# Kernel optimization log

Hardware: AMD Instinct MI355X
Metric: run time of the kernel (lower is better)

Reference implementation:

```python
import jax, jax.numpy as jnp
import numpy as np

B, S, HID = 1, 4096, 1024
NH, HD = 16, 64            # heads, per-head dim
BS = 256                    # block size
PB = 256                    # position buckets (= max_relative_positions)
EPS = 1e-7


def make_log_bucket_position(rel, num_buckets, max_position):
    sign = jnp.sign(rel)
    max_exact = num_buckets // 2
    in_exact = (rel < max_exact) & (rel > -max_exact)
    abs_pos = jnp.where(in_exact, max_exact - 1, jnp.abs(rel))
    x = jnp.log((max_position - 1) / max_exact)
    xx = jnp.log(abs_pos / max_exact) / x
    log_pos = jnp.ceil(xx * (max_exact - 1)) + max_exact
    return jnp.where(abs_pos <= max_exact, rel, (log_pos * sign).astype(jnp.int32)).astype(jnp.int32)


def split_into_blocks(x, block_size, axis):
    # [..., S, ...] -> [..., S//bs, bs, ...]; S assumed divisible by bs
    shp = x.shape
    new = shp[:axis] + (shp[axis] // block_size, block_size) + shp[axis + 1:]
    return x.reshape(new)


def concat_3_blocks(x, block_axis, seq_axis, pad_value=0):
    # pad one zero block on each side of the block axis, then concat
    # [prev, cur, next] along the within-block seq axis.
    pad = [(0, 0)] * x.ndim
    pad[block_axis] = (1, 1)
    xp = jnp.pad(x, pad, constant_values=pad_value)
    nb = x.shape[block_axis]
    slices = [jax.lax.dynamic_slice_in_dim(xp, i, nb, block_axis) for i in range(3)]
    return jnp.concatenate(slices, axis=seq_axis)


def layer_norm(x, scale, bias):
    mu = jnp.mean(x, axis=-1, keepdims=True)
    var = jnp.mean(jnp.square(x - mu), axis=-1, keepdims=True)
    return (x - mu) * jax.lax.rsqrt(var + EPS) * scale + bias


def setup_inputs() -> dict:
    key = jax.random.key(0)
    ks = jax.random.split(key, 8)
    d = {
        'hidden_states': jax.random.normal(ks[0], (B, S, HID), jnp.float32) * 0.02,
        'rel_pos_embeddings': jax.random.normal(ks[1], (S, HID), jnp.float32) * 0.02,
        'Wq': jax.random.normal(ks[2], (HID, HID), jnp.float32) * 0.01,
        'bq': jnp.zeros((HID,), jnp.float32),
        'Wk': jax.random.normal(ks[3], (HID, HID), jnp.float32) * 0.01,
        'bk': jnp.zeros((HID,), jnp.float32),
        'Wv': jax.random.normal(ks[4], (HID, HID), jnp.float32) * 0.01,
        'bv': jnp.zeros((HID,), jnp.float32),
        'Wo': jax.random.normal(ks[5], (HID, HID), jnp.float32) * 0.01,
        'bo': jnp.zeros((HID,), jnp.float32),
        'ln_scale': jnp.ones((HID,), jnp.float32),
        'ln_bias': jnp.zeros((HID,), jnp.float32),
    }
    return d


def reference(hidden_states, rel_pos_embeddings, Wq, bq, Wk, bk, Wv, bv, Wo, bo, ln_scale, ln_bias):
    b, s, hid = hidden_states.shape

    def heads(x):
        return x.reshape(x.shape[:-1] + (NH, HD))

    # content projections -> [B, nb, bs, h, d]
    q = split_into_blocks(heads(hidden_states @ Wq + bq), BS, axis=1)
    k = split_into_blocks(heads(hidden_states @ Wk + bk), BS, axis=1)
    v = split_into_blocks(heads(hidden_states @ Wv + bv), BS, axis=1)
    k3 = concat_3_blocks(k, block_axis=1, seq_axis=2)   # [B, nb, 3bs, h, d]
    v3 = concat_3_blocks(v, block_axis=1, seq_axis=2)

    c2c = jnp.einsum('bnqhd,bnkhd->bnhqk', q, k3)

    # position projections, stacked over batch (size-1 batch dim broadcasts in einsum)
    pos_q = split_into_blocks(heads(rel_pos_embeddings @ Wq + bq)[None], BS, axis=1)  # [1, nb, bs, h, d]
    pos_k = split_into_blocks(heads(rel_pos_embeddings @ Wk + bk)[None], BS, axis=1)
    pos_k3 = concat_3_blocks(pos_k, block_axis=1, seq_axis=2)                          # [1, nb, 3bs, h, d]

    rel = jnp.arange(BS, dtype=jnp.int32)[:, None] - jnp.arange(3 * BS, dtype=jnp.int32)[None, :]
    rel = make_log_bucket_position(rel, PB, PB)
    idx = jnp.clip(rel + PB, 0, 2 * PB - 1)            # [bs, 3bs]

    c2p = jnp.einsum('bnqhd,bnkhd->bnhqk', q, pos_k3)  # [B, nb, h, bs, 3bs]
    # faithful to the source: axis-less jnp.take gathers from the FLATTENED
    # score tensor -> [bs, 3bs] bias broadcast over (batch, block, head)
    c2p_bias = jnp.take(c2p, idx)

    p2c = jnp.einsum('bnqhd,bnkhd->bnhqk', pos_q, k3)
    p2c_bias = jnp.take(p2c, idx)

    scale = jnp.sqrt(jnp.asarray(HD * 3, hidden_states.dtype))
    attn = (c2c + c2p_bias + p2c_bias) / scale
    probs = jax.nn.softmax(attn, axis=-1)

    ctx = jnp.einsum('bnhqk,bnkhd->bnqhd', probs, v3)  # [B, nb, bs, h, d]
    ctx = ctx.reshape(b, s, hid)
    out = ctx @ Wo + bo
    return layer_norm(out + hidden_states, ln_scale, ln_bias)
```

## Files before the change

kernel.cpp:

```cpp
#include <hip/hip_runtime.h>
#include <stdint.h>

typedef unsigned short u16;
typedef __bf16 bf16_t;
typedef bf16_t v8bf __attribute__((ext_vector_type(8)));
typedef float v4f __attribute__((ext_vector_type(4)));

#define SEQ   4096
#define HIDN  1024
#define NHEAD 16
#define HDIM  64
#define BLK   256
#define NBLK  16

#define GLOAD_LDS16(g, l) __builtin_amdgcn_global_load_lds( \
  (const __attribute__((address_space(1))) unsigned*)(g), \
  (__attribute__((address_space(3))) unsigned*)(l), 16, 0, 0)

__device__ __forceinline__ u16 f2bf(float f){
  union { __bf16 b; u16 u; } v; v.b = (__bf16)f;
  return v.u;
}
__device__ __forceinline__ float bf2f(u16 h){
  union { unsigned u; float f; } v; v.u = ((unsigned)h) << 16;
  return v.f;
}
__device__ __forceinline__ unsigned packbf(float a, float b){
  unsigned r;
  asm("v_cvt_pk_bf16_f32 %0, %1, %2" : "=v"(r) : "v"(a), "v"(b));
  return r;
}

__global__ __launch_bounds__(256) void k_prep(const float* __restrict__ hidden, u16* __restrict__ hb,
    const float* __restrict__ Wq, const float* __restrict__ Wk,
    const float* __restrict__ Wv, const float* __restrict__ Wo, u16* __restrict__ Wt,
    const float* __restrict__ bq, const float* __restrict__ bk, const float* __restrict__ bv,
    float* __restrict__ bcat,
    const float* __restrict__ rpe, float* __restrict__ posk, float* __restrict__ posq0)
{
  __shared__ float t[32][33];
  __shared__ float red[4][64];
  int b = blockIdx.x, tid = threadIdx.x;
  if (b < 4096){
    int w = b >> 10, tile = b & 1023;
    int k0 = (tile & 31) * 32, n0 = (tile >> 5) * 32;
    const float* W = (w == 0) ? Wq : (w == 1) ? Wk : (w == 2) ? Wv : Wo;
    u16* outp = Wt + (size_t)w * 1024 * 1024;
    int x = tid & 31, y = tid >> 5;
    #pragma unroll
    for (int yy = 0; yy < 32; yy += 8) t[y + yy][x] = W[(size_t)(k0 + y + yy) * 1024 + n0 + x];
    __syncthreads();
    #pragma unroll
    for (int yy = 0; yy < 32; yy += 8) outp[(size_t)(n0 + y + yy) * 1024 + k0 + x] = f2bf(t[x][y + yy]);
  } else if (b < 4608){
    int base = (b - 4096) * 8192;
    #pragma unroll
    for (int j = 0; j < 8; j++){
      int i = base + j * 1024 + tid * 4;
      float4 f = *(const float4*)&hidden[i];
      uint2 p; p.x = packbf(f.x, f.y); p.y = packbf(f.z, f.w);
      *(uint2*)&hb[i] = p;
    }
  } else if (b == 4608){
    #pragma unroll
    for (int j = 0; j < 12; j++){
      int i = j * 256 + tid;
      const float* src = i < 1024 ? bq : (i < 2048 ? bk : bv);
      bcat[i] = src[i & 1023];
    }
  } else {
    int pb = b - 4609;
    int d = tid & 63, part = tid >> 6;
    const float* W  = (pb < 256) ? Wk : Wq;
    const float* rv = (pb < 256) ? &rpe[(size_t)pb * 1024] : rpe;
    float s = 0.f;
    for (int k = part * 256; k < part * 256 + 256; k++) s += rv[k] * W[(size_t)k * 1024 + d];
    red[part][d] = s;
    __syncthreads();
    if (part == 0){
      s = red[0][d] + red[1][d] + red[2][d] + red[3][d];
      if (pb < 256) posk[pb * 64 + d] = s + bk[d];
      else          posq0[d] = s + bq[d];
    }
  }
}

__global__ __launch_bounds__(256) void k_gemm_qkv(const u16* __restrict__ A, const u16* __restrict__ Bt,
                                                  const float* __restrict__ bias,
                                                  u16* __restrict__ qk, u16* __restrict__ Vt)
{
  __shared__ alignas(16) u16 As[2][128 * 32];
  __shared__ alignas(16) u16 Bs[2][128 * 32];
  int tid = threadIdx.x, lane = tid & 63, wid = tid >> 6;
  int wr = wid >> 1, wc = wid & 1;
  int m0 = blockIdx.y * 128, n0 = blockIdx.x * 128;
  const int K = 1024;

  v4f acc[4][4];
  #pragma unroll
  for (int m = 0; m < 4; m++)
    #pragma unroll
    for (int n = 0; n < 4; n++) acc[m][n] = (v4f){0.f, 0.f, 0.f, 0.f};

  int r = lane & 15, g = lane >> 4;
  int ob0 = wid * 2048;
  int o0  = ob0 + lane * 16;
  int row0 = o0 >> 6, col0 = (o0 & 63) >> 1;
  int row1 = (o0 + 1024) >> 6, col1 = ((o0 + 1024) & 63) >> 1;

  GLOAD_LDS16(&A [(size_t)(m0 + row0) * K + col0], &As[0][ob0 >> 1]);
  GLOAD_LDS16(&Bt[(size_t)(n0 + row0) * K + col0], &Bs[0][ob0 >> 1]);
  GLOAD_LDS16(&A [(size_t)(m0 + row1) * K + col1], &As[0][(ob0 + 1024) >> 1]);
  GLOAD_LDS16(&Bt[(size_t)(n0 + row1) * K + col1], &Bs[0][(ob0 + 1024) >> 1]);
  __syncthreads();

  int cur = 0;
  for (int kt = 0; kt < K - 32; kt += 32){
    int nx = cur ^ 1, kn = kt + 32;
    GLOAD_LDS16(&A [(size_t)(m0 + row0) * K + kn + col0], &As[nx][ob0 >> 1]);
    GLOAD_LDS16(&Bt[(size_t)(n0 + row0) * K + kn + col0], &Bs[nx][ob0 >> 1]);
    GLOAD_LDS16(&A [(size_t)(m0 + row1) * K + kn + col1], &As[nx][(ob0 + 1024) >> 1]);
    GLOAD_LDS16(&Bt[(size_t)(n0 + row1) * K + kn + col1], &Bs[nx][(ob0 + 1024) >> 1]);

    v8bf a[4], bb[4];
    #pragma unroll
    for (int m = 0; m < 4; m++) a[m] = *(const v8bf*)&As[cur][(wr * 64 + m * 16 + r) * 32 + g * 8];
    #pragma unroll
    for (int n = 0; n < 4; n++) bb[n] = *(const v8bf*)&Bs[cur][(wc * 64 + n * 16 + r) * 32 + g * 8];
    #pragma unroll
    for (int m = 0; m < 4; m++)
      #pragma unroll
      for (int n = 0; n < 4; n++)
        acc[m][n] = __builtin_amdgcn_mfma_f32_16x16x32_bf16(a[m], bb[n], acc[m][n], 0, 0, 0);
    __syncthreads();
    cur = nx;
  }
  {
    v8bf a[4], bb[4];
    #pragma unroll
    for (int m = 0; m < 4; m++) a[m] = *(const v8bf*)&As[cur][(wr * 64 + m * 16 + r) * 32 + g * 8];
    #pragma unroll
    for (int n = 0; n < 4; n++) bb[n] = *(const v8bf*)&Bs[cur][(wc * 64 + n * 16 + r) * 32 + g * 8];
    #pragma unroll
    for (int m = 0; m < 4; m++)
      #pragma unroll
      for (int n = 0; n < 4; n++)
        acc[m][n] = __builtin_amdgcn_mfma_f32_16x16x32_bf16(a[m], bb[n], acc[m][n], 0, 0, 0);
  }

  #pragma unroll
  for (int m = 0; m < 4; m++)
    #pragma unroll
    for (int n = 0; n < 4; n++){
      int col = n0 + wc * 64 + n * 16 + r;
      float bv = bias[col];
      if (n0 < 2048){
        #pragma unroll
        for (int i = 0; i < 4; i++){
          int row = m0 + wr * 64 + m * 16 + g * 4 + i;
          qk[(size_t)row * 2048 + col] = f2bf(acc[m][n][i] + bv);
        }
      } else {
        uint2 pk;
        pk.x = packbf(acc[m][n][0] + bv, acc[m][n][1] + bv);
        pk.y = packbf(acc[m][n][2] + bv, acc[m][n][3] + bv);
        int row = m0 + wr * 64 + m * 16 + g * 4;
        *(uint2*)&Vt[(size_t)(col - 2048) * 4096 + row] = pk;
      }
    }
}

__global__ __launch_bounds__(256) void k_gemm_out(const u16* __restrict__ A, const u16* __restrict__ Bt,
                                                  const float* __restrict__ bias,
                                                  const float* __restrict__ resid, float* __restrict__ Cout)
{
  __shared__ alignas(16) u16 As[2][128 * 32];
  __shared__ alignas(16) u16 Bs[2][128 * 32];
  int tid = threadIdx.x, lane = tid & 63, wid = tid >> 6;
  int wr = wid >> 1, wc = wid & 1;
  int m0 = blockIdx.y * 128, n0 = blockIdx.x * 128;
  const int K = 1024;

  v4f acc[4][4];
  #pragma unroll
  for (int m = 0; m < 4; m++)
    #pragma unroll
    for (int n = 0; n < 4; n++) acc[m][n] = (v4f){0.f, 0.f, 0.f, 0.f};

  int r = lane & 15, g = lane >> 4;
  int ob0 = wid * 2048;
  int o0  = ob0 + lane * 16;
  int row0 = o0 >> 6, col0 = (o0 & 63) >> 1;
  int row1 = (o0 + 1024) >> 6, col1 = ((o0 + 1024) & 63) >> 1;

  GLOAD_LDS16(&A [(size_t)(m0 + row0) * K + col0], &As[0][ob0 >> 1]);
  GLOAD_LDS16(&Bt[(size_t)(n0 + row0) * K + col0], &Bs[0][ob0 >> 1]);
  GLOAD_LDS16(&A [(size_t)(m0 + row1) * K + col1], &As[0][(ob0 + 1024) >> 1]);
  GLOAD_LDS16(&Bt[(size_t)(n0 + row1) * K + col1], &Bs[0][(ob0 + 1024) >> 1]);
  __syncthreads();

  int cur = 0;
  for (int kt = 0; kt < K - 32; kt += 32){
    int nx = cur ^ 1, kn = kt + 32;
    GLOAD_LDS16(&A [(size_t)(m0 + row0) * K + kn + col0], &As[nx][ob0 >> 1]);
    GLOAD_LDS16(&Bt[(size_t)(n0 + row0) * K + kn + col0], &Bs[nx][ob0 >> 1]);
    GLOAD_LDS16(&A [(size_t)(m0 + row1) * K + kn + col1], &As[nx][(ob0 + 1024) >> 1]);
    GLOAD_LDS16(&Bt[(size_t)(n0 + row1) * K + kn + col1], &Bs[nx][(ob0 + 1024) >> 1]);

    v8bf a[4], bb[4];
    #pragma unroll
    for (int m = 0; m < 4; m++) a[m] = *(const v8bf*)&As[cur][(wr * 64 + m * 16 + r) * 32 + g * 8];
    #pragma unroll
    for (int n = 0; n < 4; n++) bb[n] = *(const v8bf*)&Bs[cur][(wc * 64 + n * 16 + r) * 32 + g * 8];
    #pragma unroll
    for (int m = 0; m < 4; m++)
      #pragma unroll
      for (int n = 0; n < 4; n++)
        acc[m][n] = __builtin_amdgcn_mfma_f32_16x16x32_bf16(a[m], bb[n], acc[m][n], 0, 0, 0);
    __syncthreads();
    cur = nx;
  }
  {
    v8bf a[4], bb[4];
    #pragma unroll
    for (int m = 0; m < 4; m++) a[m] = *(const v8bf*)&As[cur][(wr * 64 + m * 16 + r) * 32 + g * 8];
    #pragma unroll
    for (int n = 0; n < 4; n++) bb[n] = *(const v8bf*)&Bs[cur][(wc * 64 + n * 16 + r) * 32 + g * 8];
    #pragma unroll
    for (int m = 0; m < 4; m++)
      #pragma unroll
      for (int n = 0; n < 4; n++)
        acc[m][n] = __builtin_amdgcn_mfma_f32_16x16x32_bf16(a[m], bb[n], acc[m][n], 0, 0, 0);
  }

  #pragma unroll
  for (int m = 0; m < 4; m++)
    #pragma unroll
    for (int n = 0; n < 4; n++){
      int col = n0 + wc * 64 + n * 16 + r;
      float bv = bias[col];
      #pragma unroll
      for (int i = 0; i < 4; i++){
        int row = m0 + wr * 64 + m * 16 + g * 4 + i;
        Cout[(size_t)row * 1024 + col] = acc[m][n][i] + bv + resid[(size_t)row * 1024 + col];
      }
    }
}

__global__ __launch_bounds__(256) void k_brow(const u16* __restrict__ qk,
                                              const float* __restrict__ posk, const float* __restrict__ posq0,
                                              float* __restrict__ brow)
{
  int b = blockIdx.x, tid = threadIdx.x;
  if (tid < 32) brow[b * 32 + tid] = 0.f;
  int u = b * 32 + (tid >> 3), sub = tid & 7;
  float c2p = 0.f, p2c = 0.f;
  #pragma unroll
  for (int j = 0; j < 8; j++){
    int d = sub * 8 + j;
    c2p += bf2f(qk[d]) * posk[u * 64 + d];
    p2c += posq0[d] * bf2f(qk[(size_t)u * 2048 + 1024 + d]);
  }
  float v = c2p + p2c;
  v += __shfl_xor(v, 1);
  v += __shfl_xor(v, 2);
  v += __shfl_xor(v, 4);
  if (sub == 0) brow[256 + u] = v;
}

__global__ void k_biasd(const float* __restrict__ brow, float* __restrict__ biasd)
{
  int t = blockIdx.x * blockDim.x + threadIdx.x;
  int rel = t - 767;
  int bucket;
  bool in_exact = (rel < 128) && (rel > -128);
  int abs_pos = in_exact ? 127 : (rel < 0 ? -rel : rel);
  if (abs_pos <= 128) bucket = rel;
  else {
    float xx = logf((float)abs_pos * (1.0f / 128.0f)) / logf(255.0f / 128.0f);
    float lp = ceilf(xx * 127.0f) + 128.0f;
    int sgn = (rel > 0) ? 1 : ((rel < 0) ? -1 : 0);
    bucket = (int)lp * sgn;
  }
  int idx = bucket + 256;
  idx = idx < 0 ? 0 : (idx > 511 ? 511 : idx);
  biasd[t] = brow[idx];
}

__global__ __launch_bounds__(256) void k_attn(const u16* __restrict__ qk, const u16* __restrict__ Vt,
                                              const float* __restrict__ biasd, u16* __restrict__ ctxg)
{
  __shared__ alignas(16) u16 Ks[128 * 64];
  __shared__ alignas(16) u16 Vs[64 * 128];
  __shared__ float bias_s[1024];

  int b = blockIdx.x;
  int h = b & 15, tile = b >> 4;
  int n = tile >> 2, qb0 = (tile & 3) * 64;
  int tid = threadIdx.x, lane = tid & 63, w = tid >> 6;
  int q0 = tile * 64;
  int g0 = (n - 1) * 256;
  const float c1 = 0.07216878364870323f * 1.4426950408889634f;
  int r = lane & 15, g = lane >> 4;

  *(float4*)&bias_s[tid * 4] = *(const float4*)&biasd[tid * 4];

  v8bf qfrag[2];
  {
    const u16* src = &qk[(size_t)(q0 + w * 16 + r) * 2048 + h * 64 + g * 8];
    qfrag[0] = *(const v8bf*)&src[0];
    qfrag[1] = *(const v8bf*)&src[32];
  }

  float mrun = -3.0e38f, lrun = 0.f;
  v4f pacc[4];
  #pragma unroll
  for (int nn = 0; nn < 4; nn++) pacc[nn] = (v4f){0.f,0.f,0.f,0.f};

  int idxA = r + ((g & 1) << 5);
  int idxB = idxA + 16;
  int myrnd = g >> 1;

  for (int c = 0; c < 6; ++c){
    int cb = g0 + c * 128;
    bool oob = (cb < 0) || (cb >= SEQ);
    if (!oob){
      #pragma unroll
      for (int t = 0; t < 4; ++t){
        int row = w * 32 + t * 8 + (lane >> 3);
        int p = lane & 7;
        GLOAD_LDS16(&qk[(size_t)(cb + row) * 2048 + 1024 + h * 64 + ((p ^ (row & 7)) * 8)],
                    Ks + (size_t)(w * 32 + t * 8) * 64);
      }
      #pragma unroll
      for (int t = 0; t < 4; ++t){
        int d = w * 16 + t * 4 + (lane >> 4);
        int p = lane & 15;
        GLOAD_LDS16(&Vt[(size_t)(h * 64 + d) * 4096 + cb + ((p ^ (d & 7)) * 8)],
                    Vs + (size_t)(w * 16 + t * 4) * 128);
      }
    }
    __syncthreads();

    v4f sacc[8];
    #pragma unroll
    for (int t = 0; t < 8; t++) sacc[t] = (v4f){0.f,0.f,0.f,0.f};
    if (!oob){
      #pragma unroll
      for (int ks = 0; ks < 2; ++ks){
        #pragma unroll
        for (int t = 0; t < 8; t++){
          int kr = t * 16 + r;
          v8bf kf = *(const v8bf*)&Ks[kr * 64 + (((4 * ks + g) ^ (kr & 7)) * 8)];
          sacc[t] = __builtin_amdgcn_mfma_f32_16x16x32_bf16(kf, qfrag[ks], sacc[t], 0, 0, 0);
        }
      }
    }

    float sv[8][4];
    float cmax = -3.0e38f;
    int ib = qb0 + w * 16 + r + 767 - c * 128 - g * 4;
    #pragma unroll
    for (int t = 0; t < 8; t++){
      #pragma unroll
      for (int i = 0; i < 4; i++)
        sv[t][i] = (sacc[t][i] + bias_s[ib - t * 16 - i]) * c1;
      float m01 = fmaxf(sv[t][0], sv[t][1]);
      float m23 = fmaxf(sv[t][2], sv[t][3]);
      cmax = fmaxf(cmax, fmaxf(m01, m23));
    }
    cmax = fmaxf(cmax, __shfl_xor(cmax, 16));
    cmax = fmaxf(cmax, __shfl_xor(cmax, 32));
    if (!__all(cmax <= mrun + 8.f)){
      float mn = fmaxf(mrun, cmax);
      float sc = exp2f(mrun - mn);
      mrun = mn;
      lrun *= sc;
      #pragma unroll
      for (int i = 0; i < 4; i++){
        float sci = __shfl(sc, (g << 2) + i);
        #pragma unroll
        for (int nn = 0; nn < 4; nn++) pacc[nn][i] *= sci;
      }
    }

    unsigned pk0[8], pk1[8];
    #pragma unroll
    for (int t = 0; t < 8; t++){
      float p0 = exp2f(sv[t][0] - mrun);
      float p1 = exp2f(sv[t][1] - mrun);
      float p2 = exp2f(sv[t][2] - mrun);
      float p3 = exp2f(sv[t][3] - mrun);
      lrun += (p0 + p1) + (p2 + p3);
      pk0[t] = packbf(p0, p1);
      pk1[t] = packbf(p2, p3);
    }

    if (!oob){
      #pragma unroll
      for (int bb4 = 0; bb4 < 4; ++bb4){
        unsigned s0a = 0, s1a = 0, s0b = 0, s1b = 0;
        #pragma unroll
        for (int rnd = 0; rnd < 2; ++rnd){
          int t = 2 * bb4 + rnd;
          unsigned ta0 = __shfl(pk0[t], idxA);
          unsigned ta1 = __shfl(pk1[t], idxA);
          unsigned tb0 = __shfl(pk0[t], idxB);
          unsigned tb1 = __shfl(pk1[t], idxB);
          if (myrnd == rnd){ s0a = ta0; s1a = ta1; s0b = tb0; s1b = tb1; }
        }
        union { unsigned u[4]; v8bf v; } af;
        af.u[0] = s0a; af.u[1] = s1a; af.u[2] = s0b; af.u[3] = s1b;
        #pragma unroll
        for (int nn = 0; nn < 4; nn++){
          int d = nn * 16 + r;
          v8bf vb = *(const v8bf*)&Vs[d * 128 + (((4 * bb4 + g) ^ (d & 7)) * 8)];
          pacc[nn] = __builtin_amdgcn_mfma_f32_16x16x32_bf16(af.v, vb, pacc[nn], 0, 0, 0);
        }
      }
    }
    __syncthreads();
  }

  lrun += __shfl_xor(lrun, 16);
  lrun += __shfl_xor(lrun, 32);
  float inv = 1.0f / lrun;
  #pragma unroll
  for (int nn = 0; nn < 4; nn++){
    int d = nn * 16 + r;
    #pragma unroll
    for (int i = 0; i < 4; i++){
      float invi = __shfl(inv, (g << 2) + i);
      int qrow = q0 + w * 16 + g * 4 + i;
      ctxg[(size_t)qrow * 1024 + h * 64 + d] = f2bf(pacc[nn][i] * invi);
    }
  }
}

__global__ __launch_bounds__(256) void k_ln(float* __restrict__ out,
                                            const float* __restrict__ gamma, const float* __restrict__ beta)
{
  __shared__ float red[8];
  int row = blockIdx.x, tid = threadIdx.x;
  int lane = tid & 63, wid = tid >> 6;
  size_t base = (size_t)row * 1024 + tid * 4;
  float4 xv = *(const float4*)&out[base];
  float v0 = xv.x, v1 = xv.y, v2 = xv.z, v3 = xv.w;
  float s = v0 + v1 + v2 + v3;
  float q = v0 * v0 + v1 * v1 + v2 * v2 + v3 * v3;
  #pragma unroll
  for (int o = 32; o; o >>= 1){ s += __shfl_down(s, o); q += __shfl_down(q, o); }
  if (lane == 0){ red[wid] = s; red[4 + wid] = q; }
  __syncthreads();
  float ts = red[0] + red[1] + red[2] + red[3];
  float tq = red[4] + red[5] + red[6] + red[7];
  float mu = ts * (1.0f / 1024.0f);
  float var = tq * (1.0f / 1024.0f) - mu * mu;
  float rstd = rsqrtf(var + 1e-7f);
  int c = tid * 4;
  out[base + 0] = (v0 - mu) * rstd * gamma[c + 0] + beta[c + 0];
  out[base + 1] = (v1 - mu) * rstd * gamma[c + 1] + beta[c + 1];
  out[base + 2] = (v2 - mu) * rstd * gamma[c + 2] + beta[c + 2];
  out[base + 3] = (v3 - mu) * rstd * gamma[c + 3] + beta[c + 3];
}

extern "C" void kernel_launch(void* const* d_in, const int* in_sizes, int n_in,
                              void* d_out, int out_size, void* d_ws, size_t ws_size,
                              hipStream_t stream)
{
  const float* hidden = (const float*)d_in[0];
  const float* rpe    = (const float*)d_in[1];
  const float* Wq = (const float*)d_in[2];
  const float* bq = (const float*)d_in[3];
  const float* Wk = (const float*)d_in[4];
  const float* bk = (const float*)d_in[5];
  const float* Wv = (const float*)d_in[6];
  const float* bv = (const float*)d_in[7];
  const float* Wo = (const float*)d_in[8];
  const float* bo = (const float*)d_in[9];
  const float* lns = (const float*)d_in[10];
  const float* lnb = (const float*)d_in[11];
  float* out = (float*)d_out;

  char* ws = (char*)d_ws;
  size_t off = 0;
  auto alloc = [&](size_t bytes){ void* p = ws + off; off += (bytes + 255) & ~(size_t)255; return p; };
  u16* hb      = (u16*)alloc((size_t)SEQ * HIDN * 2);
  u16* Wt      = (u16*)alloc((size_t)4 * HIDN * HIDN * 2);
  u16* qk      = (u16*)alloc((size_t)SEQ * 2048 * 2);
  u16* Vt      = (u16*)alloc((size_t)HIDN * SEQ * 2);
  u16* ctxb    = (u16*)alloc((size_t)SEQ * HIDN * 2);
  float* bcat  = (float*)alloc(3072 * 4);
  float* poskf = (float*)alloc(256 * 64 * 4);
  float* posq0 = (float*)alloc(64 * 4);
  float* brow  = (float*)alloc(512 * 4);
  float* biasd = (float*)alloc(1024 * 4);
  (void)ws_size; (void)in_sizes; (void)n_in; (void)out_size;

  k_prep<<<4866, 256, 0, stream>>>(hidden, hb, Wq, Wk, Wv, Wo, Wt,
                                   bq, bk, bv, bcat, rpe, poskf, posq0);

  k_gemm_qkv<<<dim3(24, 32), 256, 0, stream>>>(hb, Wt, bcat, qk, Vt);

  k_brow<<<8, 256, 0, stream>>>(qk, poskf, posq0, brow);
  k_biasd<<<4, 256, 0, stream>>>(brow, biasd);

  k_attn<<<64 * NHEAD, 256, 0, stream>>>(qk, Vt, biasd, ctxb);

  k_gemm_out<<<dim3(8, 32), 256, 0, stream>>>(ctxb, Wt + (size_t)3 * HIDN * HIDN, bo, hidden, out);

  k_ln<<<SEQ, 256, 0, stream>>>(out, lns, lnb);
}
```

Baseline: 144.3 us.

## Switch attention kernel to 32x32x16 MFMA with 128-query tiles and permlane swaps

Rewrites the attention kernel to use 32x32x16 bf16 MFMA instead of 16x16x32. Each wave now owns 32 query rows, so a block covers 128 queries and the grid halves. The P-to-A-operand transpose uses v_permlane32_swap instead of four shuffles plus selects. The scale is folded into the bias table so each score needs only one fma, and s_setprio is raised around the MFMA loops. The aim is fewer K/V tile loads per query and less shuffle and ALU overhead, at the cost of more accumulator registers per wave and fewer blocks to spread across the CUs.

```diff
diff --git a/kernel.cpp b/kernel.cpp
--- a/kernel.cpp
+++ b/kernel.cpp
@@ -5,6 +5,7 @@
 typedef __bf16 bf16_t;
 typedef bf16_t v8bf __attribute__((ext_vector_type(8)));
 typedef float v4f __attribute__((ext_vector_type(4)));
+typedef float f32x16 __attribute__((ext_vector_type(16)));
 
 #define SEQ   4096
 #define HIDN  1024
@@ -270,6 +271,7 @@
 
 __global__ void k_biasd(const float* __restrict__ brow, float* __restrict__ biasd)
 {
+  const float c1 = 0.07216878364870323f * 1.4426950408889634f;
   int t = blockIdx.x * blockDim.x + threadIdx.x;
   int rel = t - 767;
   int bucket;
@@ -284,7 +286,7 @@
   }
   int idx = bucket + 256;
   idx = idx < 0 ? 0 : (idx > 511 ? 511 : idx);
-  biasd[t] = brow[idx];
+  biasd[t] = brow[idx] * c1;
 }
 
 __global__ __launch_bounds__(256) void k_attn(const u16* __restrict__ qk, const u16* __restrict__ Vt,
@@ -296,30 +298,24 @@
 
   int b = blockIdx.x;
   int h = b & 15, tile = b >> 4;
-  int n = tile >> 2, qb0 = (tile & 3) * 64;
+  int n = tile >> 1, qb0 = (tile & 1) * 128;
   int tid = threadIdx.x, lane = tid & 63, w = tid >> 6;
-  int q0 = tile * 64;
+  int q0 = tile * 128;
   int g0 = (n - 1) * 256;
   const float c1 = 0.07216878364870323f * 1.4426950408889634f;
-  int r = lane & 15, g = lane >> 4;
+  int ql = lane & 31, hi = lane >> 5;
 
   *(float4*)&bias_s[tid * 4] = *(const float4*)&biasd[tid * 4];
 
-  v8bf qfrag[2];
-  {
-    const u16* src = &qk[(size_t)(q0 + w * 16 + r) * 2048 + h * 64 + g * 8];
-    qfrag[0] = *(const v8bf*)&src[0];
-    qfrag[1] = *(const v8bf*)&src[32];
-  }
+  v8bf qfrag[4];
+  #pragma unroll
+  for (int ks = 0; ks < 4; ks++)
+    qfrag[ks] = *(const v8bf*)&qk[(size_t)(q0 + w * 32 + ql) * 2048 + h * 64 + ks * 16 + hi * 8];
 
   float mrun = -3.0e38f, lrun = 0.f;
-  v4f pacc[4];
-  #pragma unroll
-  for (int nn = 0; nn < 4; nn++) pacc[nn] = (v4f){0.f,0.f,0.f,0.f};
-
-  int idxA = r + ((g & 1) << 5);
-  int idxB = idxA + 16;
-  int myrnd = g >> 1;
+  f32x16 pacc[2];
+  #pragma unroll
+  for (int reg = 0; reg < 16; reg++){ pacc[0][reg] = 0.f; pacc[1][reg] = 0.f; }
 
   for (int c = 0; c < 6; ++c){
     int cb = g0 + c * 128;
@@ -342,34 +338,37 @@
     }
     __syncthreads();
 
-    v4f sacc[8];
-    #pragma unroll
-    for (int t = 0; t < 8; t++) sacc[t] = (v4f){0.f,0.f,0.f,0.f};
+    f32x16 acc[4];
+    #pragma unroll
+    for (int t = 0; t < 4; t++)
+      #pragma unroll
+      for (int reg = 0; reg < 16; reg++) acc[t][reg] = 0.f;
     if (!oob){
-      #pragma unroll
-      for (int ks = 0; ks < 2; ++ks){
+      __builtin_amdgcn_s_setprio(1);
+      #pragma unroll
+      for (int ks = 0; ks < 4; ++ks){
         #pragma unroll
-        for (int t = 0; t < 8; t++){
-          int kr = t * 16 + r;
-          v8bf kf = *(const v8bf*)&Ks[kr * 64 + (((4 * ks + g) ^ (kr & 7)) * 8)];
-          sacc[t] = __builtin_amdgcn_mfma_f32_16x16x32_bf16(kf, qfrag[ks], sacc[t], 0, 0, 0);
+        for (int t = 0; t < 4; t++){
+          int kr = t * 32 + ql;
+          int slot = (ks * 2 + hi) ^ (kr & 7);
+          v8bf kf = *(const v8bf*)&Ks[kr * 64 + slot * 8];
+          acc[t] = __builtin_amdgcn_mfma_f32_32x32x16_bf16(kf, qfrag[ks], acc[t], 0, 0, 0);
         }
       }
-    }
-
-    float sv[8][4];
+      __builtin_amdgcn_s_setprio(0);
+    }
+
     float cmax = -3.0e38f;
-    int ib = qb0 + w * 16 + r + 767 - c * 128 - g * 4;
-    #pragma unroll
-    for (int t = 0; t < 8; t++){
-      #pragma unroll
-      for (int i = 0; i < 4; i++)
-        sv[t][i] = (sacc[t][i] + bias_s[ib - t * 16 - i]) * c1;
-      float m01 = fmaxf(sv[t][0], sv[t][1]);
-      float m23 = fmaxf(sv[t][2], sv[t][3]);
-      cmax = fmaxf(cmax, fmaxf(m01, m23));
-    }
-    cmax = fmaxf(cmax, __shfl_xor(cmax, 16));
+    int B0 = qb0 + w * 32 + ql + 767 - c * 128 - 4 * hi;
+    #pragma unroll
+    for (int t = 0; t < 4; t++){
+      #pragma unroll
+      for (int reg = 0; reg < 16; reg++){
+        float s = fmaf(acc[t][reg], c1, bias_s[B0 - t * 32 - (reg & 3) - 8 * (reg >> 2)]);
+        acc[t][reg] = s;
+        cmax = fmaxf(cmax, s);
+      }
+    }
     cmax = fmaxf(cmax, __shfl_xor(cmax, 32));
     if (!__all(cmax <= mrun + 8.f)){
       float mn = fmaxf(mrun, cmax);
@@ -377,63 +376,63 @@
       mrun = mn;
       lrun *= sc;
       #pragma unroll
-      for (int i = 0; i < 4; i++){
-        float sci = __shfl(sc, (g << 2) + i);
+      for (int reg = 0; reg < 16; reg++){
+        int qreg = (reg & 3) + 8 * (reg >> 2) + 4 * hi;
+        float scq = __shfl(sc, qreg);
+        pacc[0][reg] *= scq;
+        pacc[1][reg] *= scq;
+      }
+    }
+
+    unsigned pks[4][4][2];
+    #pragma unroll
+    for (int t = 0; t < 4; t++){
+      #pragma unroll
+      for (int a = 0; a < 4; a++){
+        float e0 = exp2f(acc[t][4 * a + 0] - mrun);
+        float e1 = exp2f(acc[t][4 * a + 1] - mrun);
+        float e2 = exp2f(acc[t][4 * a + 2] - mrun);
+        float e3 = exp2f(acc[t][4 * a + 3] - mrun);
+        lrun += (e0 + e1) + (e2 + e3);
+        pks[t][a][0] = packbf(e0, e1);
+        pks[t][a][1] = packbf(e2, e3);
+      }
+    }
+
+    if (!oob){
+      __builtin_amdgcn_s_setprio(1);
+      #pragma unroll
+      for (int ks16 = 0; ks16 < 8; ++ks16){
+        int t = ks16 >> 1, s = ks16 & 1;
+        unsigned u0 = pks[t][2 * s][0], v0 = pks[t][2 * s + 1][0];
+        unsigned u1 = pks[t][2 * s][1], v1 = pks[t][2 * s + 1][1];
+        asm volatile("v_permlane32_swap_b32 %0, %1" : "+v"(u0), "+v"(v0));
+        asm volatile("v_permlane32_swap_b32 %0, %1" : "+v"(u1), "+v"(v1));
+        union { unsigned u[4]; v8bf v; } af;
+        af.u[0] = u0; af.u[1] = u1; af.u[2] = v0; af.u[3] = v1;
         #pragma unroll
-        for (int nn = 0; nn < 4; nn++) pacc[nn][i] *= sci;
-      }
-    }
-
-    unsigned pk0[8], pk1[8];
-    #pragma unroll
-    for (int t = 0; t < 8; t++){
-      float p0 = exp2f(sv[t][0] - mrun);
-      float p1 = exp2f(sv[t][1] - mrun);
-      float p2 = exp2f(sv[t][2] - mrun);
-      float p3 = exp2f(sv[t][3] - mrun);
-      lrun += (p0 + p1) + (p2 + p3);
-      pk0[t] = packbf(p0, p1);
-      pk1[t] = packbf(p2, p3);
-    }
-
-    if (!oob){
-      #pragma unroll
-      for (int bb4 = 0; bb4 < 4; ++bb4){
-        unsigned s0a = 0, s1a = 0, s0b = 0, s1b = 0;
-        #pragma unroll
-        for (int rnd = 0; rnd < 2; ++rnd){
-          int t = 2 * bb4 + rnd;
-          unsigned ta0 = __shfl(pk0[t], idxA);
-          unsigned ta1 = __shfl(pk1[t], idxA);
-          unsigned tb0 = __shfl(pk0[t], idxB);
-          unsigned tb1 = __shfl(pk1[t], idxB);
-          if (myrnd == rnd){ s0a = ta0; s1a = ta1; s0b = tb0; s1b = tb1; }
+        for (int dt = 0; dt < 2; dt++){
+          int d = dt * 32 + ql;
+          int slot = (ks16 * 2 + hi) ^ (d & 7);
+          v8bf vb = *(const v8bf*)&Vs[d * 128 + slot * 8];
+          pacc[dt] = __builtin_amdgcn_mfma_f32_32x32x16_bf16(af.v, vb, pacc[dt], 0, 0, 0);
         }
-        union { unsigned u[4]; v8bf v; } af;
-        af.u[0] = s0a; af.u[1] = s1a; af.u[2] = s0b; af.u[3] = s1b;
-        #pragma unroll
-        for (int nn = 0; nn < 4; nn++){
-          int d = nn * 16 + r;
-          v8bf vb = *(const v8bf*)&Vs[d * 128 + (((4 * bb4 + g) ^ (d & 7)) * 8)];
-          pacc[nn] = __builtin_amdgcn_mfma_f32_16x16x32_bf16(af.v, vb, pacc[nn], 0, 0, 0);
-        }
-      }
+      }
+      __builtin_amdgcn_s_setprio(0);
     }
     __syncthreads();
   }
 
-  lrun += __shfl_xor(lrun, 16);
   lrun += __shfl_xor(lrun, 32);
   float inv = 1.0f / lrun;
   #pragma unroll
-  for (int nn = 0; nn < 4; nn++){
-    int d = nn * 16 + r;
-    #pragma unroll
-    for (int i = 0; i < 4; i++){
-      float invi = __shfl(inv, (g << 2) + i);
-      int qrow = q0 + w * 16 + g * 4 + i;
-      ctxg[(size_t)qrow * 1024 + h * 64 + d] = f2bf(pacc[nn][i] * invi);
-    }
+  for (int reg = 0; reg < 16; reg++){
+    int qreg = (reg & 3) + 8 * (reg >> 2) + 4 * hi;
+    float invq = __shfl(inv, qreg);
+    int qrow = q0 + w * 32 + qreg;
+    #pragma unroll
+    for (int dt = 0; dt < 2; dt++)
+      ctxg[(size_t)qrow * 1024 + h * 64 + dt * 32 + ql] = f2bf(pacc[dt][reg] * invq);
   }
 }
 
@@ -505,7 +504,7 @@
   k_brow<<<8, 256, 0, stream>>>(qk, poskf, posq0, brow);
   k_biasd<<<4, 256, 0, stream>>>(brow, biasd);
 
-  k_attn<<<64 * NHEAD, 256, 0, stream>>>(qk, Vt, biasd, ctxb);
+  k_attn<<<32 * NHEAD, 256, 0, stream>>>(qk, Vt, biasd, ctxb);
 
   k_gemm_out<<<dim3(8, 32), 256, 0, stream>>>(ctxb, Wt + (size_t)3 * HIDN * HIDN, bo, hidden, out);
 
```

New measurement: 150.8 us. +4.5%, slower.
